# Performance work log

Measured on AMD Instinct MI355X. Metric: run time of the kernel, lower is better.

The kernel has to match this reference:

```python
import jax, jax.numpy as jnp
import numpy as np

G = 32       # normal clusters
F = 256      # features per normal cluster
H = 52       # ceil(0.2*256)
O = 5        # normal_group_hidden
UF = 512     # unique (-1) cluster features
UH = 103     # ceil(0.2*512)
UO = 20      # 5*4
B = 8192


def setup_inputs() -> dict:
    key = jax.random.key(0)
    ks = jax.random.split(key, 16)
    s = lambda fan_in: 1.0 / np.sqrt(fan_in)
    return {
        "x": jax.random.normal(ks[0], (B, G * F + UF), dtype=jnp.float32),
        # grouped (block-diagonal) head weights for the 32 identical normal clusters
        "W1": jax.random.uniform(ks[1], (G, F, H), jnp.float32, -s(F), s(F)),
        "b1": jax.random.uniform(ks[2], (G, H), jnp.float32, -s(F), s(F)),
        "W2": jax.random.uniform(ks[3], (G, H, H), jnp.float32, -s(H), s(H)),
        "b2": jax.random.uniform(ks[4], (G, H), jnp.float32, -s(H), s(H)),
        "W3": jax.random.uniform(ks[5], (G, H, O), jnp.float32, -s(H), s(H)),
        "b3": jax.random.uniform(ks[6], (G, O), jnp.float32, -s(H), s(H)),
        # unique cluster_id=-1 head
        "uW1": jax.random.uniform(ks[7], (UF, UH), jnp.float32, -s(UF), s(UF)),
        "ub1": jax.random.uniform(ks[8], (UH,), jnp.float32, -s(UF), s(UF)),
        "uW2": jax.random.uniform(ks[9], (UH, UH), jnp.float32, -s(UH), s(UH)),
        "ub2": jax.random.uniform(ks[10], (UH,), jnp.float32, -s(UH), s(UH)),
        "uW3": jax.random.uniform(ks[11], (UH, UO), jnp.float32, -s(UH), s(UH)),
        "ub3": jax.random.uniform(ks[12], (UH,), jnp.float32, -s(UH), s(UH))[:UO],
        # final linear (bias=False): in = G*O + UO = 180
        "outW": jax.random.uniform(ks[13], (G * O + UO,), jnp.float32,
                                    -s(G * O + UO), s(G * O + UO)),
    }


def reference(x, W1, b1, W2, b2, W3, b3, uW1, ub1, uW2, ub2, uW3, ub3, outW):
    act = jax.nn.elu
    # --- grouped heads: [B, G, F] block-diagonal MLPs (dropout=identity in eval)
    xg = x[:, : G * F].reshape(B, G, F)
    h = act(jnp.einsum("bgf,gfh->bgh", xg, W1) + b1)
    h = act(jnp.einsum("bgh,ghk->bgk", h, W2) + b2)
    h = act(jnp.einsum("bgh,gho->bgo", h, W3) + b3)      # [B, G, O]
    head_norm = h.reshape(B, G * O)
    # --- unique (-1) head
    u = x[:, G * F :]
    u = act(u @ uW1 + ub1)
    u = act(u @ uW2 + ub2)
    u = act(u @ uW3 + ub3)                                # [B, UO]
    head_outs = jnp.concatenate([head_norm, u], axis=1)   # [B, 180]
    return head_outs @ outW                               # [B]
```

## Files before the change

### kernel.cpp

```cpp
#include <hip/hip_runtime.h>
#include <hip/hip_bf16.h>

typedef short v8s __attribute__((ext_vector_type(8)));
typedef float v4f __attribute__((ext_vector_type(4)));

#define MFMA_B16(A, B, C) __builtin_amdgcn_mfma_f32_16x16x32_bf16((A), (B), (C), 0, 0, 0)

#define NB   8192
#define XW   8704
#define GF   256
#define GH   52
#define GO   5
#define UFK  512
#define UHN  103
#define UON  20

__device__ __forceinline__ unsigned short f2bf(float f) {
  union { __hip_bfloat16 h; unsigned short u; } cv;
  cv.h = __float2bfloat16(f);
  return cv.u;
}

__device__ __forceinline__ float elu1(float y) {
  return y > 0.f ? y : (__expf(y) - 1.f);
}

__device__ __forceinline__ v8s pack8(const float* p) {
  float4 q0 = *(const float4*)p;
  float4 q1 = *(const float4*)(p + 4);
  v8s a;
  a[0] = (short)f2bf(q0.x); a[1] = (short)f2bf(q0.y);
  a[2] = (short)f2bf(q0.z); a[3] = (short)f2bf(q0.w);
  a[4] = (short)f2bf(q1.x); a[5] = (short)f2bf(q1.y);
  a[6] = (short)f2bf(q1.z); a[7] = (short)f2bf(q1.w);
  return a;
}

__global__ __launch_bounds__(256) void group_kernel(
    const float* __restrict__ x,  const float* __restrict__ W1,
    const float* __restrict__ b1, const float* __restrict__ W2,
    const float* __restrict__ b2, const float* __restrict__ W3,
    const float* __restrict__ b3, const float* __restrict__ outW,
    float* __restrict__ out)
{
  const int g    = blockIdx.y;
  const int row0 = blockIdx.x * 64;
  const int tid  = threadIdx.x;
  const int wave = tid >> 6;
  const int lane = tid & 63;
  const int l15  = lane & 15;
  const int l4   = lane >> 4;

  __shared__ __align__(16) unsigned short w1t[64 * 264];
  __shared__ __align__(16) unsigned short w2t[64 * 72];
  __shared__ __align__(16) unsigned short w3t[16 * 72];
  __shared__ __align__(16) unsigned short hbuf[4][16 * 72];
  __shared__ float bias1[64], bias2[64], bias3[16];

  {
    unsigned int* p1 = (unsigned int*)w1t;
    for (int i = tid; i < 64 * 264 / 2; i += 256) p1[i] = 0u;
    unsigned int* p2 = (unsigned int*)w2t;
    for (int i = tid; i < 64 * 72 / 2; i += 256) p2[i] = 0u;
    unsigned int* p3 = (unsigned int*)w3t;
    for (int i = tid; i < 16 * 72 / 2; i += 256) p3[i] = 0u;
  }
  __syncthreads();

  for (int i = tid; i < GF * GH; i += 256) {
    int f = i / GH, h = i % GH;
    w1t[h * 264 + f] = f2bf(W1[g * (GF * GH) + i]);
  }
  for (int i = tid; i < GH * GH; i += 256) {
    int h = i / GH, k = i % GH;
    w2t[k * 72 + h] = f2bf(W2[g * (GH * GH) + i]);
  }
  for (int i = tid; i < GH * GO; i += 256) {
    int h = i / GO, o = i % GO;
    w3t[o * 72 + h] = f2bf(W3[g * (GH * GO) + i]);
  }
  if (tid < 64)        { bias1[tid] = (tid < GH) ? b1[g * GH + tid] : 0.f; }
  else if (tid < 128)  { int c = tid - 64;  bias2[c] = (c < GH) ? b2[g * GH + c] : 0.f; }
  else if (tid < 144)  { int c = tid - 128; bias3[c] = (c < GO) ? b3[g * GO + c] : 0.f; }
  __syncthreads();

  const int  row  = row0 + wave * 16 + l15;
  const float* xrow = x + (long)row * XW + g * GF;

  const v4f z = {0.f, 0.f, 0.f, 0.f};

  v4f acc1[4] = {z, z, z, z};
#pragma unroll
  for (int kk = 0; kk < 8; ++kk) {
    v8s a = pack8(xrow + kk * 32 + l4 * 8);
#pragma unroll
    for (int n = 0; n < 4; ++n) {
      v8s b = *(const v8s*)&w1t[(n * 16 + l15) * 264 + kk * 32 + l4 * 8];
      acc1[n] = MFMA_B16(a, b, acc1[n]);
    }
  }
#pragma unroll
  for (int n = 0; n < 4; ++n) {
    int col = n * 16 + l15;
    float bb = bias1[col];
#pragma unroll
    for (int r = 0; r < 4; ++r) {
      float h = elu1(acc1[n][r] + bb);
      hbuf[wave][(l4 * 4 + r) * 72 + col] = f2bf(h);
    }
  }
  __syncthreads();

  v4f acc2[4] = {z, z, z, z};
#pragma unroll
  for (int kk = 0; kk < 2; ++kk) {
    v8s a = *(const v8s*)&hbuf[wave][l15 * 72 + kk * 32 + l4 * 8];
#pragma unroll
    for (int n = 0; n < 4; ++n) {
      v8s b = *(const v8s*)&w2t[(n * 16 + l15) * 72 + kk * 32 + l4 * 8];
      acc2[n] = MFMA_B16(a, b, acc2[n]);
    }
  }
  __syncthreads();
#pragma unroll
  for (int n = 0; n < 4; ++n) {
    int col = n * 16 + l15;
    float bb = bias2[col];
#pragma unroll
    for (int r = 0; r < 4; ++r) {
      float h = elu1(acc2[n][r] + bb);
      hbuf[wave][(l4 * 4 + r) * 72 + col] = f2bf(h);
    }
  }
  __syncthreads();

  v4f acc3 = z;
#pragma unroll
  for (int kk = 0; kk < 2; ++kk) {
    v8s a = *(const v8s*)&hbuf[wave][l15 * 72 + kk * 32 + l4 * 8];
    v8s b = *(const v8s*)&w3t[l15 * 72 + kk * 32 + l4 * 8];
    acc3 = MFMA_B16(a, b, acc3);
  }

  float ow = (l15 < GO) ? outW[g * GO + l15] : 0.f;
  float bb = bias3[l15];
  float v0 = elu1(acc3[0] + bb) * ow;
  float v1 = elu1(acc3[1] + bb) * ow;
  float v2 = elu1(acc3[2] + bb) * ow;
  float v3 = elu1(acc3[3] + bb) * ow;
#pragma unroll
  for (int off = 1; off < 16; off <<= 1) {
    v0 += __shfl_xor(v0, off, 64);
    v1 += __shfl_xor(v1, off, 64);
    v2 += __shfl_xor(v2, off, 64);
    v3 += __shfl_xor(v3, off, 64);
  }
  if (l15 < 4) {
    float val = (l15 == 0) ? v0 : (l15 == 1) ? v1 : (l15 == 2) ? v2 : v3;
    atomicAdd(&out[row0 + wave * 16 + l4 * 4 + l15], val);
  }
}

__global__ __launch_bounds__(128) void universal_kernel(
    const float* __restrict__ x,   const float* __restrict__ uW1,
    const float* __restrict__ ub1, const float* __restrict__ uW2,
    const float* __restrict__ ub2, const float* __restrict__ uW3,
    const float* __restrict__ ub3, const float* __restrict__ outW,
    float* __restrict__ out)
{
  const int row0 = blockIdx.x * 32;
  const int tid  = threadIdx.x;
  const int wave = tid >> 6;
  const int lane = tid & 63;
  const int l15  = lane & 15;
  const int l4   = lane >> 4;

  __shared__ __align__(16) unsigned short wub[128 * 136];
  __shared__ __align__(16) unsigned short hbufu[2][16 * 136];
  __shared__ float biasu[128];

  {
    unsigned int* p = (unsigned int*)wub;
    for (int i = tid; i < 128 * 136 / 2; i += 128) p[i] = 0u;
  }
  biasu[tid] = (tid < UHN) ? ub1[tid] : 0.f;
  __syncthreads();

  const int  row  = row0 + wave * 16 + l15;
  const float* xrow = x + (long)row * XW + 8192;

  const v4f z = {0.f, 0.f, 0.f, 0.f};

  v4f acc1[8] = {z, z, z, z, z, z, z, z};
  for (int c = 0; c < 4; ++c) {
    for (int i = tid; i < 128 * UHN; i += 128) {
      int kl = i / UHN, h = i % UHN;
      wub[h * 136 + kl] = f2bf(uW1[(c * 128 + kl) * UHN + h]);
    }
    __syncthreads();
#pragma unroll
    for (int kk = 0; kk < 4; ++kk) {
      v8s a = pack8(xrow + c * 128 + kk * 32 + l4 * 8);
#pragma unroll
      for (int n = 0; n < 8; ++n) {
        v8s b = *(const v8s*)&wub[(n * 16 + l15) * 136 + kk * 32 + l4 * 8];
        acc1[n] = MFMA_B16(a, b, acc1[n]);
      }
    }
    __syncthreads();
  }
#pragma unroll
  for (int n = 0; n < 8; ++n) {
    int col = n * 16 + l15;
    float bb = biasu[col];
#pragma unroll
    for (int r = 0; r < 4; ++r) {
      float h = elu1(acc1[n][r] + bb);
      hbufu[wave][(l4 * 4 + r) * 136 + col] = f2bf(h);
    }
  }
  __syncthreads();

  for (int i = tid; i < UHN * UHN; i += 128) {
    int h = i / UHN, k = i % UHN;
    wub[k * 136 + h] = f2bf(uW2[i]);
  }
  biasu[tid] = (tid < UHN) ? ub2[tid] : 0.f;
  __syncthreads();

  v4f acc2[8] = {z, z, z, z, z, z, z, z};
#pragma unroll
  for (int kk = 0; kk < 4; ++kk) {
    v8s a = *(const v8s*)&hbufu[wave][l15 * 136 + kk * 32 + l4 * 8];
#pragma unroll
    for (int n = 0; n < 8; ++n) {
      v8s b = *(const v8s*)&wub[(n * 16 + l15) * 136 + kk * 32 + l4 * 8];
      acc2[n] = MFMA_B16(a, b, acc2[n]);
    }
  }
  __syncthreads();
#pragma unroll
  for (int n = 0; n < 8; ++n) {
    int col = n * 16 + l15;
    float bb = biasu[col];
#pragma unroll
    for (int r = 0; r < 4; ++r) {
      float h = elu1(acc2[n][r] + bb);
      hbufu[wave][(l4 * 4 + r) * 136 + col] = f2bf(h);
    }
  }
  __syncthreads();

  {
    unsigned int* p = (unsigned int*)(wub + 20 * 136);
    for (int i = tid; i < 12 * 136 / 2; i += 128) p[i] = 0u;
  }
  for (int i = tid; i < UHN * UON; i += 128) {
    int h = i / UON, o = i % UON;
    wub[o * 136 + h] = f2bf(uW3[i]);
  }
  if (tid < 32) biasu[tid] = (tid < UON) ? ub3[tid] : 0.f;
  __syncthreads();

  v4f acc3[2] = {z, z};
#pragma unroll
  for (int kk = 0; kk < 4; ++kk) {
    v8s a = *(const v8s*)&hbufu[wave][l15 * 136 + kk * 32 + l4 * 8];
#pragma unroll
    for (int n = 0; n < 2; ++n) {
      v8s b = *(const v8s*)&wub[(n * 16 + l15) * 136 + kk * 32 + l4 * 8];
      acc3[n] = MFMA_B16(a, b, acc3[n]);
    }
  }

  float ow0 = (l15 < UON)      ? outW[160 + l15]      : 0.f;
  float ow1 = (16 + l15 < UON) ? outW[160 + 16 + l15] : 0.f;
  float bb0 = biasu[l15];
  float bb1 = biasu[16 + l15];
  float v0 = elu1(acc3[0][0] + bb0) * ow0 + elu1(acc3[1][0] + bb1) * ow1;
  float v1 = elu1(acc3[0][1] + bb0) * ow0 + elu1(acc3[1][1] + bb1) * ow1;
  float v2 = elu1(acc3[0][2] + bb0) * ow0 + elu1(acc3[1][2] + bb1) * ow1;
  float v3 = elu1(acc3[0][3] + bb0) * ow0 + elu1(acc3[1][3] + bb1) * ow1;
#pragma unroll
  for (int off = 1; off < 16; off <<= 1) {
    v0 += __shfl_xor(v0, off, 64);
    v1 += __shfl_xor(v1, off, 64);
    v2 += __shfl_xor(v2, off, 64);
    v3 += __shfl_xor(v3, off, 64);
  }
  if (l15 < 4) {
    float val = (l15 == 0) ? v0 : (l15 == 1) ? v1 : (l15 == 2) ? v2 : v3;
    atomicAdd(&out[row0 + wave * 16 + l4 * 4 + l15], val);
  }
}

extern "C" void kernel_launch(void* const* d_in, const int* in_sizes, int n_in,
                              void* d_out, int out_size, void* d_ws, size_t ws_size,
                              hipStream_t stream) {
  const float* x    = (const float*)d_in[0];
  const float* W1   = (const float*)d_in[1];
  const float* b1   = (const float*)d_in[2];
  const float* W2   = (const float*)d_in[3];
  const float* b2   = (const float*)d_in[4];
  const float* W3   = (const float*)d_in[5];
  const float* b3   = (const float*)d_in[6];
  const float* uW1  = (const float*)d_in[7];
  const float* ub1  = (const float*)d_in[8];
  const float* uW2  = (const float*)d_in[9];
  const float* ub2  = (const float*)d_in[10];
  const float* uW3  = (const float*)d_in[11];
  const float* ub3  = (const float*)d_in[12];
  const float* outW = (const float*)d_in[13];
  float* out = (float*)d_out;

  hipMemsetAsync(out, 0, (size_t)out_size * sizeof(float), stream);

  dim3 ggrid(NB / 64, 32);
  group_kernel<<<ggrid, 256, 0, stream>>>(x, W1, b1, W2, b2, W3, b3, outW, out);
  universal_kernel<<<NB / 32, 128, 0, stream>>>(x, uW1, ub1, uW2, ub2, uW3, ub3, outW, out);
}
```

Baseline: 558.9 us.

## Pre-convert weights once and fuse group and unique heads into persistent kernel

Adds a prep kernel that converts and transposes all weights into a padded bf16 workspace once per call. The two head kernels become one launch of 576 blocks. Group blocks stage their bf16 weights into shared memory with vector copies and loop over 8 row tiles each. Unique-head blocks read weights straight from global or L2. This removes the per-block scalar transpose-and-convert work that the old code repeated across 4096 group blocks and 256 unique blocks, and it merges the two launches. The risks are lower parallelism, since the grid is now persistent, and uncached global reads of B fragments in the unique path.

```diff
diff --git a/kernel.cpp b/kernel.cpp
--- a/kernel.cpp
+++ b/kernel.cpp
@@ -8,12 +8,14 @@
 
 #define NB   8192
 #define XW   8704
-#define GF   256
-#define GH   52
-#define GO   5
-#define UFK  512
-#define UHN  103
-#define UON  20
+
+#define GW1     16896
+#define GW12    21504
+#define GW_STRIDE 22656
+#define OFF_U1  724992
+#define OFF_U2  791552
+#define OFF_U3  808960
+#define WS_TOTAL 813312
 
 __device__ __forceinline__ unsigned short f2bf(float f) {
   union { __hip_bfloat16 h; unsigned short u; } cv;
@@ -36,261 +38,221 @@
   return a;
 }
 
-__global__ __launch_bounds__(256) void group_kernel(
-    const float* __restrict__ x,  const float* __restrict__ W1,
-    const float* __restrict__ b1, const float* __restrict__ W2,
-    const float* __restrict__ b2, const float* __restrict__ W3,
-    const float* __restrict__ b3, const float* __restrict__ outW,
+__global__ __launch_bounds__(256) void prep_kernel(
+    const float* __restrict__ W1, const float* __restrict__ W2,
+    const float* __restrict__ W3, const float* __restrict__ uW1,
+    const float* __restrict__ uW2, const float* __restrict__ uW3,
+    unsigned short* __restrict__ ws16)
+{
+  int i = blockIdx.x * 256 + threadIdx.x;
+  if (i >= WS_TOTAL) return;
+  float val = 0.f;
+  if (i < OFF_U1) {
+    int g = i / GW_STRIDE, r = i % GW_STRIDE;
+    if (r < GW1)        { int h = r / 264, f = r % 264;            if (h < 52 && f < 256) val = W1[(g * 256 + f) * 52 + h]; }
+    else if (r < GW12)  { int r2 = r - GW1;  int k = r2 / 72, h = r2 % 72; if (k < 52 && h < 52) val = W2[g * 2704 + h * 52 + k]; }
+    else                { int r3 = r - GW12; int o = r3 / 72, h = r3 % 72; if (o < 5  && h < 52) val = W3[g * 260 + h * 5 + o]; }
+  } else if (i < OFF_U2) {
+    int j = i - OFF_U1; int h = j / 520, k = j % 520; if (h < 103 && k < 512) val = uW1[k * 103 + h];
+  } else if (i < OFF_U3) {
+    int j = i - OFF_U2; int k2 = j / 136, h = j % 136; if (k2 < 103 && h < 103) val = uW2[h * 103 + k2];
+  } else {
+    int j = i - OFF_U3; int o = j / 136, h = j % 136; if (o < 20 && h < 103) val = uW3[h * 20 + o];
+  }
+  ws16[i] = f2bf(val);
+}
+
+__global__ __launch_bounds__(256) void fused_kernel(
+    const float* __restrict__ x,
+    const unsigned short* __restrict__ ws16,
+    const float* __restrict__ b1, const float* __restrict__ b2,
+    const float* __restrict__ b3,
+    const float* __restrict__ ub1, const float* __restrict__ ub2,
+    const float* __restrict__ ub3,
+    const float* __restrict__ outW,
     float* __restrict__ out)
 {
-  const int g    = blockIdx.y;
-  const int row0 = blockIdx.x * 64;
+  __shared__ __align__(16) unsigned char smem[55104];
+
+  const int bid  = blockIdx.x;
   const int tid  = threadIdx.x;
   const int wave = tid >> 6;
   const int lane = tid & 63;
   const int l15  = lane & 15;
   const int l4   = lane >> 4;
-
-  __shared__ __align__(16) unsigned short w1t[64 * 264];
-  __shared__ __align__(16) unsigned short w2t[64 * 72];
-  __shared__ __align__(16) unsigned short w3t[16 * 72];
-  __shared__ __align__(16) unsigned short hbuf[4][16 * 72];
-  __shared__ float bias1[64], bias2[64], bias3[16];
+  const v4f z = {0.f, 0.f, 0.f, 0.f};
+
+  if (bid < 64) {
+    const unsigned short* u1 = ws16 + OFF_U1;
+    const unsigned short* u2 = ws16 + OFF_U2;
+    const unsigned short* u3 = ws16 + OFF_U3;
+    unsigned short* hbufu = (unsigned short*)smem + wave * 2176;
+
+    for (int tt = 0; tt < 2; ++tt) {
+      const int rowbase = bid * 128 + wave * 32 + tt * 16;
+      const float* xrow = x + (size_t)(rowbase + l15) * XW + 8192;
+
+      v4f acc1[8] = {z, z, z, z, z, z, z, z};
+#pragma unroll 4
+      for (int kk = 0; kk < 16; ++kk) {
+        v8s a = pack8(xrow + kk * 32 + l4 * 8);
+#pragma unroll
+        for (int n = 0; n < 8; ++n) {
+          v8s b = *(const v8s*)&u1[(n * 16 + l15) * 520 + kk * 32 + l4 * 8];
+          acc1[n] = MFMA_B16(a, b, acc1[n]);
+        }
+      }
+#pragma unroll
+      for (int n = 0; n < 8; ++n) {
+        int col = n * 16 + l15;
+        float bb = (col < 103) ? ub1[col] : 0.f;
+#pragma unroll
+        for (int r = 0; r < 4; ++r)
+          hbufu[(l4 * 4 + r) * 136 + col] = f2bf(elu1(acc1[n][r] + bb));
+      }
+
+      v4f acc2[8] = {z, z, z, z, z, z, z, z};
+#pragma unroll
+      for (int kk = 0; kk < 4; ++kk) {
+        v8s a = *(const v8s*)&hbufu[l15 * 136 + kk * 32 + l4 * 8];
+#pragma unroll
+        for (int n = 0; n < 8; ++n) {
+          v8s b = *(const v8s*)&u2[(n * 16 + l15) * 136 + kk * 32 + l4 * 8];
+          acc2[n] = MFMA_B16(a, b, acc2[n]);
+        }
+      }
+#pragma unroll
+      for (int n = 0; n < 8; ++n) {
+        int col = n * 16 + l15;
+        float bb = (col < 103) ? ub2[col] : 0.f;
+#pragma unroll
+        for (int r = 0; r < 4; ++r)
+          hbufu[(l4 * 4 + r) * 136 + col] = f2bf(elu1(acc2[n][r] + bb));
+      }
+
+      v4f acc3[2] = {z, z};
+#pragma unroll
+      for (int kk = 0; kk < 4; ++kk) {
+        v8s a = *(const v8s*)&hbufu[l15 * 136 + kk * 32 + l4 * 8];
+#pragma unroll
+        for (int n = 0; n < 2; ++n) {
+          v8s b = *(const v8s*)&u3[(n * 16 + l15) * 136 + kk * 32 + l4 * 8];
+          acc3[n] = MFMA_B16(a, b, acc3[n]);
+        }
+      }
+
+      float ow0 = (l15 < 20)      ? outW[160 + l15]      : 0.f;
+      float ow1 = (16 + l15 < 20) ? outW[160 + 16 + l15] : 0.f;
+      float bb0 = (l15 < 20)      ? ub3[l15]             : 0.f;
+      float bb1 = (16 + l15 < 20) ? ub3[16 + l15]        : 0.f;
+      float v0 = elu1(acc3[0][0] + bb0) * ow0 + elu1(acc3[1][0] + bb1) * ow1;
+      float v1 = elu1(acc3[0][1] + bb0) * ow0 + elu1(acc3[1][1] + bb1) * ow1;
+      float v2 = elu1(acc3[0][2] + bb0) * ow0 + elu1(acc3[1][2] + bb1) * ow1;
+      float v3 = elu1(acc3[0][3] + bb0) * ow0 + elu1(acc3[1][3] + bb1) * ow1;
+#pragma unroll
+      for (int off = 1; off < 16; off <<= 1) {
+        v0 += __shfl_xor(v0, off, 64);
+        v1 += __shfl_xor(v1, off, 64);
+        v2 += __shfl_xor(v2, off, 64);
+        v3 += __shfl_xor(v3, off, 64);
+      }
+      if (l15 < 4) {
+        float val = (l15 == 0) ? v0 : (l15 == 1) ? v1 : (l15 == 2) ? v2 : v3;
+        atomicAdd(&out[rowbase + l4 * 4 + l15], val);
+      }
+    }
+    return;
+  }
+
+  const int gbid = bid - 64;
+  const int g = gbid & 31;
+  const int s = gbid >> 5;
+
+  const unsigned short* w1t = (const unsigned short*)smem;
+  const unsigned short* w2t = (const unsigned short*)(smem + 33792);
+  const unsigned short* w3t = (const unsigned short*)(smem + 43008);
+  unsigned short* hbuf = (unsigned short*)(smem + 45312) + wave * 1152;
+  float* bias1 = (float*)(smem + 54528);
+  float* bias2 = (float*)(smem + 54784);
+  float* bias3 = (float*)(smem + 55040);
 
   {
-    unsigned int* p1 = (unsigned int*)w1t;
-    for (int i = tid; i < 64 * 264 / 2; i += 256) p1[i] = 0u;
-    unsigned int* p2 = (unsigned int*)w2t;
-    for (int i = tid; i < 64 * 72 / 2; i += 256) p2[i] = 0u;
-    unsigned int* p3 = (unsigned int*)w3t;
-    for (int i = tid; i < 16 * 72 / 2; i += 256) p3[i] = 0u;
+    const v8s* wsg = (const v8s*)(ws16 + (size_t)g * GW_STRIDE);
+    v8s* sv = (v8s*)smem;
+    for (int i = tid; i < 2832; i += 256) sv[i] = wsg[i];
+    if (tid < 64)       { bias1[tid] = (tid < 52) ? b1[g * 52 + tid] : 0.f; }
+    else if (tid < 128) { int c = tid - 64;  bias2[c] = (c < 52) ? b2[g * 52 + c] : 0.f; }
+    else if (tid < 144) { int c = tid - 128; bias3[c] = (c < 5)  ? b3[g * 5 + c]  : 0.f; }
   }
   __syncthreads();
 
-  for (int i = tid; i < GF * GH; i += 256) {
-    int f = i / GH, h = i % GH;
-    w1t[h * 264 + f] = f2bf(W1[g * (GF * GH) + i]);
-  }
-  for (int i = tid; i < GH * GH; i += 256) {
-    int h = i / GH, k = i % GH;
-    w2t[k * 72 + h] = f2bf(W2[g * (GH * GH) + i]);
-  }
-  for (int i = tid; i < GH * GO; i += 256) {
-    int h = i / GO, o = i % GO;
-    w3t[o * 72 + h] = f2bf(W3[g * (GH * GO) + i]);
-  }
-  if (tid < 64)        { bias1[tid] = (tid < GH) ? b1[g * GH + tid] : 0.f; }
-  else if (tid < 128)  { int c = tid - 64;  bias2[c] = (c < GH) ? b2[g * GH + c] : 0.f; }
-  else if (tid < 144)  { int c = tid - 128; bias3[c] = (c < GO) ? b3[g * GO + c] : 0.f; }
-  __syncthreads();
-
-  const int  row  = row0 + wave * 16 + l15;
-  const float* xrow = x + (long)row * XW + g * GF;
-
-  const v4f z = {0.f, 0.f, 0.f, 0.f};
-
-  v4f acc1[4] = {z, z, z, z};
-#pragma unroll
-  for (int kk = 0; kk < 8; ++kk) {
-    v8s a = pack8(xrow + kk * 32 + l4 * 8);
+  for (int t = s; t < 128; t += 16) {
+    const int row0 = t * 64;
+    const float* xrow = x + (size_t)(row0 + wave * 16 + l15) * XW + g * 256;
+
+    v4f acc1[4] = {z, z, z, z};
+#pragma unroll
+    for (int kk = 0; kk < 8; ++kk) {
+      v8s a = pack8(xrow + kk * 32 + l4 * 8);
+#pragma unroll
+      for (int n = 0; n < 4; ++n) {
+        v8s b = *(const v8s*)&w1t[(n * 16 + l15) * 264 + kk * 32 + l4 * 8];
+        acc1[n] = MFMA_B16(a, b, acc1[n]);
+      }
+    }
 #pragma unroll
     for (int n = 0; n < 4; ++n) {
-      v8s b = *(const v8s*)&w1t[(n * 16 + l15) * 264 + kk * 32 + l4 * 8];
-      acc1[n] = MFMA_B16(a, b, acc1[n]);
-    }
-  }
-#pragma unroll
-  for (int n = 0; n < 4; ++n) {
-    int col = n * 16 + l15;
-    float bb = bias1[col];
-#pragma unroll
-    for (int r = 0; r < 4; ++r) {
-      float h = elu1(acc1[n][r] + bb);
-      hbuf[wave][(l4 * 4 + r) * 72 + col] = f2bf(h);
-    }
-  }
-  __syncthreads();
-
-  v4f acc2[4] = {z, z, z, z};
-#pragma unroll
-  for (int kk = 0; kk < 2; ++kk) {
-    v8s a = *(const v8s*)&hbuf[wave][l15 * 72 + kk * 32 + l4 * 8];
+      int col = n * 16 + l15;
+      float bb = bias1[col];
+#pragma unroll
+      for (int r = 0; r < 4; ++r)
+        hbuf[(l4 * 4 + r) * 72 + col] = f2bf(elu1(acc1[n][r] + bb));
+    }
+
+    v4f acc2[4] = {z, z, z, z};
+#pragma unroll
+    for (int kk = 0; kk < 2; ++kk) {
+      v8s a = *(const v8s*)&hbuf[l15 * 72 + kk * 32 + l4 * 8];
+#pragma unroll
+      for (int n = 0; n < 4; ++n) {
+        v8s b = *(const v8s*)&w2t[(n * 16 + l15) * 72 + kk * 32 + l4 * 8];
+        acc2[n] = MFMA_B16(a, b, acc2[n]);
+      }
+    }
 #pragma unroll
     for (int n = 0; n < 4; ++n) {
-      v8s b = *(const v8s*)&w2t[(n * 16 + l15) * 72 + kk * 32 + l4 * 8];
-      acc2[n] = MFMA_B16(a, b, acc2[n]);
-    }
-  }
-  __syncthreads();
-#pragma unroll
-  for (int n = 0; n < 4; ++n) {
-    int col = n * 16 + l15;
-    float bb = bias2[col];
-#pragma unroll
-    for (int r = 0; r < 4; ++r) {
-      float h = elu1(acc2[n][r] + bb);
-      hbuf[wave][(l4 * 4 + r) * 72 + col] = f2bf(h);
-    }
-  }
-  __syncthreads();
-
-  v4f acc3 = z;
-#pragma unroll
-  for (int kk = 0; kk < 2; ++kk) {
-    v8s a = *(const v8s*)&hbuf[wave][l15 * 72 + kk * 32 + l4 * 8];
-    v8s b = *(const v8s*)&w3t[l15 * 72 + kk * 32 + l4 * 8];
-    acc3 = MFMA_B16(a, b, acc3);
-  }
-
-  float ow = (l15 < GO) ? outW[g * GO + l15] : 0.f;
-  float bb = bias3[l15];
-  float v0 = elu1(acc3[0] + bb) * ow;
-  float v1 = elu1(acc3[1] + bb) * ow;
-  float v2 = elu1(acc3[2] + bb) * ow;
-  float v3 = elu1(acc3[3] + bb) * ow;
-#pragma unroll
-  for (int off = 1; off < 16; off <<= 1) {
-    v0 += __shfl_xor(v0, off, 64);
-    v1 += __shfl_xor(v1, off, 64);
-    v2 += __shfl_xor(v2, off, 64);
-    v3 += __shfl_xor(v3, off, 64);
-  }
-  if (l15 < 4) {
-    float val = (l15 == 0) ? v0 : (l15 == 1) ? v1 : (l15 == 2) ? v2 : v3;
-    atomicAdd(&out[row0 + wave * 16 + l4 * 4 + l15], val);
-  }
-}
-
-__global__ __launch_bounds__(128) void universal_kernel(
-    const float* __restrict__ x,   const float* __restrict__ uW1,
-    const float* __restrict__ ub1, const float* __restrict__ uW2,
-    const float* __restrict__ ub2, const float* __restrict__ uW3,
-    const float* __restrict__ ub3, const float* __restrict__ outW,
-    float* __restrict__ out)
-{
-  const int row0 = blockIdx.x * 32;
-  const int tid  = threadIdx.x;
-  const int wave = tid >> 6;
-  const int lane = tid & 63;
-  const int l15  = lane & 15;
-  const int l4   = lane >> 4;
-
-  __shared__ __align__(16) unsigned short wub[128 * 136];
-  __shared__ __align__(16) unsigned short hbufu[2][16 * 136];
-  __shared__ float biasu[128];
-
-  {
-    unsigned int* p = (unsigned int*)wub;
-    for (int i = tid; i < 128 * 136 / 2; i += 128) p[i] = 0u;
-  }
-  biasu[tid] = (tid < UHN) ? ub1[tid] : 0.f;
-  __syncthreads();
-
-  const int  row  = row0 + wave * 16 + l15;
-  const float* xrow = x + (long)row * XW + 8192;
-
-  const v4f z = {0.f, 0.f, 0.f, 0.f};
-
-  v4f acc1[8] = {z, z, z, z, z, z, z, z};
-  for (int c = 0; c < 4; ++c) {
-    for (int i = tid; i < 128 * UHN; i += 128) {
-      int kl = i / UHN, h = i % UHN;
-      wub[h * 136 + kl] = f2bf(uW1[(c * 128 + kl) * UHN + h]);
-    }
-    __syncthreads();
-#pragma unroll
-    for (int kk = 0; kk < 4; ++kk) {
-      v8s a = pack8(xrow + c * 128 + kk * 32 + l4 * 8);
-#pragma unroll
-      for (int n = 0; n < 8; ++n) {
-        v8s b = *(const v8s*)&wub[(n * 16 + l15) * 136 + kk * 32 + l4 * 8];
-        acc1[n] = MFMA_B16(a, b, acc1[n]);
-      }
-    }
-    __syncthreads();
-  }
-#pragma unroll
-  for (int n = 0; n < 8; ++n) {
-    int col = n * 16 + l15;
-    float bb = biasu[col];
-#pragma unroll
-    for (int r = 0; r < 4; ++r) {
-      float h = elu1(acc1[n][r] + bb);
-      hbufu[wave][(l4 * 4 + r) * 136 + col] = f2bf(h);
-    }
-  }
-  __syncthreads();
-
-  for (int i = tid; i < UHN * UHN; i += 128) {
-    int h = i / UHN, k = i % UHN;
-    wub[k * 136 + h] = f2bf(uW2[i]);
-  }
-  biasu[tid] = (tid < UHN) ? ub2[tid] : 0.f;
-  __syncthreads();
-
-  v4f acc2[8] = {z, z, z, z, z, z, z, z};
-#pragma unroll
-  for (int kk = 0; kk < 4; ++kk) {
-    v8s a = *(const v8s*)&hbufu[wave][l15 * 136 + kk * 32 + l4 * 8];
-#pragma unroll
-    for (int n = 0; n < 8; ++n) {
-      v8s b = *(const v8s*)&wub[(n * 16 + l15) * 136 + kk * 32 + l4 * 8];
-      acc2[n] = MFMA_B16(a, b, acc2[n]);
-    }
-  }
-  __syncthreads();
-#pragma unroll
-  for (int n = 0; n < 8; ++n) {
-    int col = n * 16 + l15;
-    float bb = biasu[col];
-#pragma unroll
-    for (int r = 0; r < 4; ++r) {
-      float h = elu1(acc2[n][r] + bb);
-      hbufu[wave][(l4 * 4 + r) * 136 + col] = f2bf(h);
-    }
-  }
-  __syncthreads();
-
-  {
-    unsigned int* p = (unsigned int*)(wub + 20 * 136);
-    for (int i = tid; i < 12 * 136 / 2; i += 128) p[i] = 0u;
-  }
-  for (int i = tid; i < UHN * UON; i += 128) {
-    int h = i / UON, o = i % UON;
-    wub[o * 136 + h] = f2bf(uW3[i]);
-  }
-  if (tid < 32) biasu[tid] = (tid < UON) ? ub3[tid] : 0.f;
-  __syncthreads();
-
-  v4f acc3[2] = {z, z};
-#pragma unroll
-  for (int kk = 0; kk < 4; ++kk) {
-    v8s a = *(const v8s*)&hbufu[wave][l15 * 136 + kk * 32 + l4 * 8];
-#pragma unroll
-    for (int n = 0; n < 2; ++n) {
-      v8s b = *(const v8s*)&wub[(n * 16 + l15) * 136 + kk * 32 + l4 * 8];
-      acc3[n] = MFMA_B16(a, b, acc3[n]);
-    }
-  }
-
-  float ow0 = (l15 < UON)      ? outW[160 + l15]      : 0.f;
-  float ow1 = (16 + l15 < UON) ? outW[160 + 16 + l15] : 0.f;
-  float bb0 = biasu[l15];
-  float bb1 = biasu[16 + l15];
-  float v0 = elu1(acc3[0][0] + bb0) * ow0 + elu1(acc3[1][0] + bb1) * ow1;
-  float v1 = elu1(acc3[0][1] + bb0) * ow0 + elu1(acc3[1][1] + bb1) * ow1;
-  float v2 = elu1(acc3[0][2] + bb0) * ow0 + elu1(acc3[1][2] + bb1) * ow1;
-  float v3 = elu1(acc3[0][3] + bb0) * ow0 + elu1(acc3[1][3] + bb1) * ow1;
-#pragma unroll
-  for (int off = 1; off < 16; off <<= 1) {
-    v0 += __shfl_xor(v0, off, 64);
-    v1 += __shfl_xor(v1, off, 64);
-    v2 += __shfl_xor(v2, off, 64);
-    v3 += __shfl_xor(v3, off, 64);
-  }
-  if (l15 < 4) {
-    float val = (l15 == 0) ? v0 : (l15 == 1) ? v1 : (l15 == 2) ? v2 : v3;
-    atomicAdd(&out[row0 + wave * 16 + l4 * 4 + l15], val);
+      int col = n * 16 + l15;
+      float bb = bias2[col];
+#pragma unroll
+      for (int r = 0; r < 4; ++r)
+        hbuf[(l4 * 4 + r) * 72 + col] = f2bf(elu1(acc2[n][r] + bb));
+    }
+
+    v4f acc3 = z;
+#pragma unroll
+    for (int kk = 0; kk < 2; ++kk) {
+      v8s a = *(const v8s*)&hbuf[l15 * 72 + kk * 32 + l4 * 8];
+      v8s b = *(const v8s*)&w3t[l15 * 72 + kk * 32 + l4 * 8];
+      acc3 = MFMA_B16(a, b, acc3);
+    }
+
+    float ow = (l15 < 5) ? outW[g * 5 + l15] : 0.f;
+    float bb = bias3[l15];
+    float v0 = elu1(acc3[0] + bb) * ow;
+    float v1 = elu1(acc3[1] + bb) * ow;
+    float v2 = elu1(acc3[2] + bb) * ow;
+    float v3 = elu1(acc3[3] + bb) * ow;
+#pragma unroll
+    for (int off = 1; off < 16; off <<= 1) {
+      v0 += __shfl_xor(v0, off, 64);
+      v1 += __shfl_xor(v1, off, 64);
+      v2 += __shfl_xor(v2, off, 64);
+      v3 += __shfl_xor(v3, off, 64);
+    }
+    if (l15 < 4) {
+      float val = (l15 == 0) ? v0 : (l15 == 1) ? v1 : (l15 == 2) ? v2 : v3;
+      atomicAdd(&out[row0 + wave * 16 + l4 * 4 + l15], val);
+    }
   }
 }
 
@@ -312,10 +274,9 @@
   const float* ub3  = (const float*)d_in[12];
   const float* outW = (const float*)d_in[13];
   float* out = (float*)d_out;
+  unsigned short* ws16 = (unsigned short*)d_ws;
 
   hipMemsetAsync(out, 0, (size_t)out_size * sizeof(float), stream);
-
-  dim3 ggrid(NB / 64, 32);
-  group_kernel<<<ggrid, 256, 0, stream>>>(x, W1, b1, W2, b2, W3, b3, outW, out);
-  universal_kernel<<<NB / 32, 128, 0, stream>>>(x, uW1, ub1, uW2, ub2, uW3, ub3, outW, out);
-}
+  prep_kernel<<<(WS_TOTAL + 255) / 256, 256, 0, stream>>>(W1, W2, W3, uW1, uW2, uW3, ws16);
+  fused_kernel<<<576, 256, 0, stream>>>(x, ws16, b1, b2, b3, ub1, ub2, ub3, outW, out);
+}
```

Result: faster. 452.4 us (-19.0%).
